# Performance work log

Measured on AMD Instinct MI355X. Metric: run time of the kernel, lower is better.

## Reference

```python
import jax, jax.numpy as jnp
import numpy as np

B, D_IN, H, C = 8192, 256, 512, 10
EXPANSION = 2
INTER = int(H * EXPANSION * 2 / 3)  # 682, matches torch int(dim*expansion*2/3)
K_OUTER, H_CYCLES, L_CYCLES = 4, 2, 3
EPS = 1e-6


def rms_norm(x):
    return x * jax.lax.rsqrt(jnp.mean(x * x, axis=-1, keepdims=True) + EPS)


def swiglu(x, Wgu, Wd):
    gate, up = jnp.split(x @ Wgu, 2, axis=-1)
    return (jax.nn.silu(gate) * up) @ Wd


def setup_inputs() -> dict:
    key = jax.random.key(0)
    ks = jax.random.split(key, 13)
    s = 0.02
    return {
        "x": jax.random.normal(ks[0], (B, D_IN), jnp.float32),
        "W_in": jax.random.normal(ks[1], (D_IN, H), jnp.float32) * s,
        "b_in": jnp.zeros((H,), jnp.float32),
        "W_fb": jax.random.normal(ks[2], (C, H), jnp.float32) * s,
        "b_fb": jnp.zeros((H,), jnp.float32),
        "Wgu1": jax.random.normal(ks[3], (H, 2 * INTER), jnp.float32) * s,
        "Wd1": jax.random.normal(ks[4], (INTER, H), jnp.float32) * s,
        "Wgu2": jax.random.normal(ks[5], (H, 2 * INTER), jnp.float32) * s,
        "Wd2": jax.random.normal(ks[6], (INTER, H), jnp.float32) * s,
        "H_init": jax.random.normal(ks[7], (H,), jnp.float32) * s,
        "L_init": jax.random.normal(ks[8], (H,), jnp.float32) * s,
        "W_out": jax.random.normal(ks[9], (H, C), jnp.float32) * s,
        "b_out": jnp.zeros((C,), jnp.float32),
    }


def reference(x, W_in, b_in, W_fb, b_fb, Wgu1, Wd1, Wgu2, Wd2,
              H_init, L_init, W_out, b_out):
    def block(h):  # TRMBlock: two post-norm SwiGLU sublayers
        h = rms_norm(h + swiglu(h, Wgu1, Wd1))
        h = rms_norm(h + swiglu(h, Wgu2, Wd2))
        return h

    def level(hidden, injection):  # TRMLevel with n_layers=1
        return block(hidden + injection)

    x_proj = x @ W_in + b_in                       # [B,H]
    z_H = jnp.broadcast_to(H_init, (x.shape[0], H))
    z_L = jnp.broadcast_to(L_init, (x.shape[0], H))
    feedback = jnp.zeros((x.shape[0], H), x.dtype)
    all_logits = []
    for k in range(K_OUTER):
        combined = x_proj + feedback
        for _h in range(H_CYCLES):
            for _l in range(L_CYCLES):
                z_L = level(z_L, z_H + combined)
            z_H = level(z_H, z_L)
        if k < K_OUTER - 1:  # grad_last_only=True: no_grad + detach
            z_H = jax.lax.stop_gradient(z_H)
            z_L = jax.lax.stop_gradient(z_L)
        logits = z_H @ W_out + b_out               # [B,C]
        all_logits.append(logits)
        probs = jax.nn.softmax(jax.lax.stop_gradient(logits), axis=-1)
        feedback = probs @ W_fb + b_fb
    return logits, jnp.stack(all_logits)
```

## Files before the change

kernel.cpp:

```cpp
#include <hip/hip_runtime.h>

#define DEVI __device__ __forceinline__

typedef __attribute__((ext_vector_type(8)))  short short8;
typedef __attribute__((ext_vector_type(4)))  short short4v;
typedef __attribute__((ext_vector_type(16))) float f32x16;

constexpr int NROW = 8192;
constexpr int HD   = 512;
constexpr int DIN  = 256;
constexpr int NC   = 10;

constexpr int NP  = 22;
constexpr int KT1 = 32;
constexpr int KT2 = 44;
constexpr int KTX = 16;
constexpr int NTH = 16;

constexpr int SZ_GU = KT1*NP*64*8;
constexpr int SZ_D  = KT2*NTH*64*8;
constexpr int SZ_IN = KTX*NTH*64*8;

DEVI short f2bf(float x){
  unsigned u = __builtin_bit_cast(unsigned, x);
  unsigned r = u + 0x7FFFu + ((u >> 16) & 1u);
  return (short)(r >> 16);
}
DEVI float bf2f(short s){
  unsigned u = ((unsigned)(unsigned short)s) << 16;
  return __builtin_bit_cast(float, u);
}
DEVI f32x16 MF(short8 a, short8 b, f32x16 c){
  return __builtin_amdgcn_mfma_f32_32x32x16_bf16(a, b, c, 0, 0, 0);
}
DEVI f32x16 fzero(){
  f32x16 v;
  #pragma unroll
  for (int i = 0; i < 16; ++i) v[i] = 0.f;
  return v;
}

struct WSet { const short *GH, *GL, *UH, *UL, *DH, *DL; };

DEVI void silu_store(int p, const f32x16& cg, const f32x16& cu,
                     short* INh_, short* INl_, int l)
{
  const int m = l & 31, g = l >> 5;
  #pragma unroll
  for (int q = 0; q < 4; ++q) {
    short4v hi, lo;
    #pragma unroll
    for (int pos = 0; pos < 4; ++pos) {
      const int r = q*4 + pos;
      float gv = cg[r], uv = cu[r];
      float sv = (gv / (1.0f + __expf(-gv))) * uv;
      short h = f2bf(sv);
      hi[pos] = h;
      lo[pos] = f2bf(sv - bf2f(h));
    }
    const int kt2  = 2*p + (q >> 1);
    const int slot = ((q & 1) << 5) + m;
    const int base = (kt2*64 + slot)*8 + (g << 2);
    *(short4v*)&INh_[base] = hi;
    *(short4v*)&INl_[base] = lo;
  }
}

template<int NPAIR>
DEVI void g1pass(int p0, const WSet& Wt,
                 const short* A1h_, const short* A1l_,
                 short* INh_, short* INl_, int l)
{
  f32x16 ag[NPAIR], au[NPAIR];
  #pragma unroll
  for (int j = 0; j < NPAIR; ++j) { ag[j] = fzero(); au[j] = fzero(); }
  const short *pGH[NPAIR], *pGL[NPAIR], *pUH[NPAIR], *pUL[NPAIR];
  #pragma unroll
  for (int j = 0; j < NPAIR; ++j) {
    const int p = p0 + 8*j;
    pGH[j] = Wt.GH + p*512 + l*8;
    pGL[j] = Wt.GL + p*512 + l*8;
    pUH[j] = Wt.UH + p*512 + l*8;
    pUL[j] = Wt.UL + p*512 + l*8;
  }
  #pragma unroll 2
  for (int kt = 0; kt < KT1; ++kt) {
    const int ab = (kt*64 + l)*8;
    short8 bh = *(const short8*)&A1h_[ab];
    short8 bl = *(const short8*)&A1l_[ab];
    const int o = kt*(NP*512);
    #pragma unroll
    for (int j = 0; j < NPAIR; ++j) {
      short8 gh = *(const short8*)(pGH[j] + o);
      short8 gl = *(const short8*)(pGL[j] + o);
      short8 uh = *(const short8*)(pUH[j] + o);
      short8 ul = *(const short8*)(pUL[j] + o);
      ag[j] = MF(gh, bh, ag[j]);
      ag[j] = MF(gl, bh, ag[j]);
      ag[j] = MF(gh, bl, ag[j]);
      au[j] = MF(uh, bh, au[j]);
      au[j] = MF(ul, bh, au[j]);
      au[j] = MF(uh, bl, au[j]);
    }
  }
  #pragma unroll
  for (int j = 0; j < NPAIR; ++j)
    silu_store(p0 + 8*j, ag[j], au[j], INh_, INl_, l);
}

DEVI void sublayer(float (&S)[32], const WSet& Wt,
                   short* A1h_, short* A1l_, short* INh_, short* INl_,
                   float* rmsS_, int w, int l)
{
  const int m = l & 31, g = l >> 5;
  #pragma unroll
  for (int t = 0; t < 2; ++t) {
    #pragma unroll
    for (int q = 0; q < 4; ++q) {
      short4v hi, lo;
      #pragma unroll
      for (int pos = 0; pos < 4; ++pos) {
        float v = S[t*16 + q*4 + pos];
        short h = f2bf(v);
        hi[pos] = h;
        lo[pos] = f2bf(v - bf2f(h));
      }
      const int kt   = 4*w + 2*t + (q >> 1);
      const int slot = ((q & 1) << 5) + m;
      const int base = (kt*64 + slot)*8 + (g << 2);
      *(short4v*)&A1h_[base] = hi;
      *(short4v*)&A1l_[base] = lo;
    }
  }
  __syncthreads();
  g1pass<2>(w, Wt, A1h_, A1l_, INh_, INl_, l);
  if (w + 16 < NP) g1pass<1>(w + 16, Wt, A1h_, A1l_, INh_, INl_, l);
  __syncthreads();
  f32x16 c0 = fzero(), c1 = fzero();
  {
    const short* d0h = Wt.DH + (2*w  )*512 + l*8;
    const short* d0l = Wt.DL + (2*w  )*512 + l*8;
    const short* d1h = Wt.DH + (2*w+1)*512 + l*8;
    const short* d1l = Wt.DL + (2*w+1)*512 + l*8;
    #pragma unroll 2
    for (int kt = 0; kt < KT2; ++kt) {
      const int ab = (kt*64 + l)*8;
      short8 bh = *(const short8*)&INh_[ab];
      short8 bl = *(const short8*)&INl_[ab];
      const int o = kt*(NTH*512);
      short8 a0h = *(const short8*)(d0h + o);
      short8 a0l = *(const short8*)(d0l + o);
      short8 a1h = *(const short8*)(d1h + o);
      short8 a1l = *(const short8*)(d1l + o);
      c0 = MF(a0h, bh, c0); c0 = MF(a0l, bh, c0); c0 = MF(a0h, bl, c0);
      c1 = MF(a1h, bh, c1); c1 = MF(a1l, bh, c1); c1 = MF(a1h, bl, c1);
    }
  }
  float ss = 0.f;
  #pragma unroll
  for (int s = 0; s < 32; ++s) {
    float y = S[s] + (s < 16 ? c0[s & 15] : c1[s & 15]);
    S[s] = y;
    ss += y*y;
  }
  ss += __shfl_xor(ss, 32);
  if (l < 32) rmsS_[w*32 + l] = ss;
  __syncthreads();
  float tot = 0.f;
  #pragma unroll
  for (int wv = 0; wv < 8; ++wv) tot += rmsS_[wv*32 + m];
  const float rinv = 1.0f / sqrtf(tot * (1.0f/512.0f) + 1e-6f);
  #pragma unroll
  for (int s = 0; s < 32; ++s) S[s] *= rinv;
}

__global__ __launch_bounds__(512, 2) void trm_main(
    const float* __restrict__ x,
    const float* __restrict__ b_in,
    const float* __restrict__ W_fb,
    const float* __restrict__ b_fb,
    const float* __restrict__ H_init,
    const float* __restrict__ L_init,
    const float* __restrict__ W_out,
    const float* __restrict__ b_out,
    float* __restrict__ xp,
    const short* __restrict__ BinH, const short* __restrict__ BinL,
    const short* __restrict__ G1H, const short* __restrict__ G1L,
    const short* __restrict__ U1H, const short* __restrict__ U1L,
    const short* __restrict__ D1H, const short* __restrict__ D1L,
    const short* __restrict__ G2H, const short* __restrict__ G2L,
    const short* __restrict__ U2H, const short* __restrict__ U2L,
    const short* __restrict__ D2H, const short* __restrict__ D2L,
    float* __restrict__ out)
{
  __shared__ alignas(16) char smem[156672];
  short* A1h  = (short*)(smem);
  short* A1l  = (short*)(smem + 32768);
  short* INh  = (short*)(smem + 65536);
  short* INl  = (short*)(smem + 110592);
  float* rmsS = (float*)(smem + 155648);
  float* lgS  = (float*)(smem);
  float* pbS  = (float*)(smem + 10240);

  const int tid = threadIdx.x;
  const int l = tid & 63;
  const int w = tid >> 6;
  const int m = l & 31;
  const int g = l >> 5;
  const int wg = blockIdx.x;
  const int row0 = wg * 32;

  float zL[32], zH[32], cb[32];

  #pragma unroll
  for (int kk = 0; kk < 2; ++kk) {
    const int kt = 2*w + kk;
    const float4* xr = (const float4*)(x + (size_t)(row0 + m)*DIN + kt*16 + g*8);
    float4 v0 = xr[0];
    float4 v1 = xr[1];
    float v[8] = {v0.x, v0.y, v0.z, v0.w, v1.x, v1.y, v1.z, v1.w};
    short8 hi, lo;
    #pragma unroll
    for (int i = 0; i < 8; ++i) {
      short h = f2bf(v[i]);
      hi[i] = h;
      lo[i] = f2bf(v[i] - bf2f(h));
    }
    const int base = (kt*64 + l)*8;
    *(short8*)&A1h[base] = hi;
    *(short8*)&A1l[base] = lo;
  }
  __syncthreads();
  {
    f32x16 c0 = fzero(), c1 = fzero();
    const short* i0h = BinH + (2*w  )*512 + l*8;
    const short* i0l = BinL + (2*w  )*512 + l*8;
    const short* i1h = BinH + (2*w+1)*512 + l*8;
    const short* i1l = BinL + (2*w+1)*512 + l*8;
    #pragma unroll 2
    for (int kt = 0; kt < KTX; ++kt) {
      const int ab = (kt*64 + l)*8;
      short8 bh = *(const short8*)&A1h[ab];
      short8 bl = *(const short8*)&A1l[ab];
      const int o = kt*(NTH*512);
      short8 a0h = *(const short8*)(i0h + o);
      short8 a0l = *(const short8*)(i0l + o);
      short8 a1h = *(const short8*)(i1h + o);
      short8 a1l = *(const short8*)(i1l + o);
      c0 = MF(a0h, bh, c0); c0 = MF(a0l, bh, c0); c0 = MF(a0h, bl, c0);
      c1 = MF(a1h, bh, c1); c1 = MF(a1l, bh, c1); c1 = MF(a1h, bl, c1);
    }
    #pragma unroll
    for (int s = 0; s < 32; ++s) {
      const int r = s & 15;
      const int cc = w*64 + (s >> 4)*32 + (r & 3) + ((r >> 2) << 3) + (g << 2);
      float v = (s < 16 ? c0[r] : c1[r]) + b_in[cc];
      cb[s] = v;
      xp[(size_t)(wg*8 + w)*2048 + s*64 + l] = v;
      zH[s] = H_init[cc];
      zL[s] = L_init[cc];
    }
  }
  __syncthreads();

  const WSet W1{G1H, G1L, U1H, U1L, D1H, D1L};
  const WSet W2{G2H, G2L, U2H, U2L, D2H, D2L};

  #pragma unroll 1
  for (int k = 0; k < 4; ++k) {
    #pragma unroll 1
    for (int hc = 0; hc < 2; ++hc) {
      #pragma unroll 1
      for (int li = 0; li < 3; ++li) {
        #pragma unroll
        for (int s = 0; s < 32; ++s) zL[s] += zH[s] + cb[s];
        #pragma unroll 1
        for (int sub = 0; sub < 2; ++sub)
          sublayer(zL, sub ? W2 : W1, A1h, A1l, INh, INl, rmsS, w, l);
      }
      #pragma unroll
      for (int s = 0; s < 32; ++s) zH[s] += zL[s];
      #pragma unroll 1
      for (int sub = 0; sub < 2; ++sub)
        sublayer(zH, sub ? W2 : W1, A1h, A1l, INh, INl, rmsS, w, l);
    }
    {
      float part[10];
      #pragma unroll
      for (int c = 0; c < NC; ++c) part[c] = 0.f;
      #pragma unroll
      for (int s = 0; s < 32; ++s) {
        const int r = s & 15;
        const int cc = w*64 + (s >> 4)*32 + (r & 3) + ((r >> 2) << 3) + (g << 2);
        const float zz = zH[s];
        #pragma unroll
        for (int c = 0; c < NC; ++c) part[c] += zz * W_out[cc*NC + c];
      }
      #pragma unroll
      for (int c = 0; c < NC; ++c) part[c] += __shfl_xor(part[c], 32);
      if (l < 32) {
        #pragma unroll
        for (int c = 0; c < NC; ++c) lgS[(w*32 + l)*NC + c] = part[c];
      }
      __syncthreads();
      if (w == 0 && l < 32) {
        float lg[10];
        #pragma unroll
        for (int c = 0; c < NC; ++c) lg[c] = b_out[c];
        #pragma unroll
        for (int wv = 0; wv < 8; ++wv) {
          #pragma unroll
          for (int c = 0; c < NC; ++c) lg[c] += lgS[(wv*32 + l)*NC + c];
        }
        const int row = row0 + l;
        #pragma unroll
        for (int c = 0; c < NC; ++c) out[(size_t)(1 + k)*81920 + row*NC + c] = lg[c];
        if (k == 3) {
          #pragma unroll
          for (int c = 0; c < NC; ++c) out[row*NC + c] = lg[c];
        }
        float mx = lg[0];
        #pragma unroll
        for (int c = 1; c < NC; ++c) mx = fmaxf(mx, lg[c]);
        float e[10], sum = 0.f;
        #pragma unroll
        for (int c = 0; c < NC; ++c) { e[c] = __expf(lg[c] - mx); sum += e[c]; }
        const float inv = 1.0f / sum;
        #pragma unroll
        for (int c = 0; c < NC; ++c) pbS[l*NC + c] = e[c] * inv;
      }
      __syncthreads();
      if (k < 3) {
        #pragma unroll
        for (int s = 0; s < 32; ++s) {
          const int r = s & 15;
          const int cc = w*64 + (s >> 4)*32 + (r & 3) + ((r >> 2) << 3) + (g << 2);
          float fb = b_fb[cc];
          #pragma unroll
          for (int c = 0; c < NC; ++c) fb += pbS[m*NC + c] * W_fb[c*HD + cc];
          cb[s] = xp[(size_t)(wg*8 + w)*2048 + s*64 + l] + fb;
        }
      }
      __syncthreads();
    }
  }
}

__global__ void prep_gu(const float* __restrict__ Wgu,
                        short* __restrict__ GH, short* __restrict__ GL,
                        short* __restrict__ UH, short* __restrict__ UL)
{
  const int t = blockIdx.x*256 + threadIdx.x;
  if (t >= 2*KT1*NP*64) return;
  const int l = t & 63;
  const int rest = t >> 6;
  const int nt = rest % NP;
  const int rest2 = rest / NP;
  const int kt = rest2 & 31;
  const int gu = rest2 >> 5;
  const int n  = nt*32 + (l & 31);
  const int kb = kt*16 + (l >> 5)*8;
  short8 hi, lo;
  #pragma unroll
  for (int i = 0; i < 8; ++i) {
    float v = 0.f;
    if (n < 682) v = Wgu[(size_t)(kb + i)*1364 + gu*682 + n];
    short h = f2bf(v);
    hi[i] = h;
    lo[i] = f2bf(v - bf2f(h));
  }
  const int base = ((kt*NP + nt)*64 + l)*8;
  short* H = gu ? UH : GH;
  short* L = gu ? UL : GL;
  *(short8*)&H[base] = hi;
  *(short8*)&L[base] = lo;
}

__global__ void prep_d(const float* __restrict__ Wd,
                       short* __restrict__ DH, short* __restrict__ DL)
{
  const int t = blockIdx.x*256 + threadIdx.x;
  if (t >= KT2*NTH*64) return;
  const int l = t & 63;
  const int rest = t >> 6;
  const int nt = rest % NTH;
  const int kt2 = rest / NTH;
  const int n  = nt*32 + (l & 31);
  const int kb = kt2*16 + (l >> 5)*8;
  short8 hi, lo;
  #pragma unroll
  for (int i = 0; i < 8; ++i) {
    const int k2 = kb + i;
    float v = (k2 < 682) ? Wd[(size_t)k2*HD + n] : 0.f;
    short h = f2bf(v);
    hi[i] = h;
    lo[i] = f2bf(v - bf2f(h));
  }
  const int base = ((kt2*NTH + nt)*64 + l)*8;
  *(short8*)&DH[base] = hi;
  *(short8*)&DL[base] = lo;
}

__global__ void prep_in(const float* __restrict__ Win,
                        short* __restrict__ IH, short* __restrict__ IL)
{
  const int t = blockIdx.x*256 + threadIdx.x;
  if (t >= KTX*NTH*64) return;
  const int l = t & 63;
  const int rest = t >> 6;
  const int nt = rest % NTH;
  const int kt = rest / NTH;
  const int n  = nt*32 + (l & 31);
  const int kb = kt*16 + (l >> 5)*8;
  short8 hi, lo;
  #pragma unroll
  for (int i = 0; i < 8; ++i) {
    float v = Win[(size_t)(kb + i)*HD + n];
    short h = f2bf(v);
    hi[i] = h;
    lo[i] = f2bf(v - bf2f(h));
  }
  const int base = ((kt*NTH + nt)*64 + l)*8;
  *(short8*)&IH[base] = hi;
  *(short8*)&IL[base] = lo;
}

extern "C" void kernel_launch(void* const* d_in, const int* in_sizes, int n_in,
                              void* d_out, int out_size, void* d_ws, size_t ws_size,
                              hipStream_t stream)
{
  const float* x     = (const float*)d_in[0];
  const float* W_in  = (const float*)d_in[1];
  const float* b_in  = (const float*)d_in[2];
  const float* W_fb  = (const float*)d_in[3];
  const float* b_fb  = (const float*)d_in[4];
  const float* Wgu1  = (const float*)d_in[5];
  const float* Wd1   = (const float*)d_in[6];
  const float* Wgu2  = (const float*)d_in[7];
  const float* Wd2   = (const float*)d_in[8];
  const float* Hini  = (const float*)d_in[9];
  const float* Lini  = (const float*)d_in[10];
  const float* W_out = (const float*)d_in[11];
  const float* b_out = (const float*)d_in[12];
  float* out = (float*)d_out;

  char* ws = (char*)d_ws;
  size_t off = 0;
  auto alloc = [&](size_t bytes) {
    char* p = ws + off;
    off = (off + bytes + 255) & ~(size_t)255;
    return p;
  };
  float* xp   = (float*)alloc((size_t)NROW*HD*4);
  short* BinH = (short*)alloc((size_t)SZ_IN*2);
  short* BinL = (short*)alloc((size_t)SZ_IN*2);
  short* G1H = (short*)alloc((size_t)SZ_GU*2); short* G1L = (short*)alloc((size_t)SZ_GU*2);
  short* U1H = (short*)alloc((size_t)SZ_GU*2); short* U1L = (short*)alloc((size_t)SZ_GU*2);
  short* D1H = (short*)alloc((size_t)SZ_D*2);  short* D1L = (short*)alloc((size_t)SZ_D*2);
  short* G2H = (short*)alloc((size_t)SZ_GU*2); short* G2L = (short*)alloc((size_t)SZ_GU*2);
  short* U2H = (short*)alloc((size_t)SZ_GU*2); short* U2L = (short*)alloc((size_t)SZ_GU*2);
  short* D2H = (short*)alloc((size_t)SZ_D*2);  short* D2L = (short*)alloc((size_t)SZ_D*2);

  const int n1 = 2*KT1*NP*64;
  prep_gu<<<(n1+255)/256, 256, 0, stream>>>(Wgu1, G1H, G1L, U1H, U1L);
  prep_gu<<<(n1+255)/256, 256, 0, stream>>>(Wgu2, G2H, G2L, U2H, U2L);
  const int n2 = KT2*NTH*64;
  prep_d<<<(n2+255)/256, 256, 0, stream>>>(Wd1, D1H, D1L);
  prep_d<<<(n2+255)/256, 256, 0, stream>>>(Wd2, D2H, D2L);
  const int n3 = KTX*NTH*64;
  prep_in<<<(n3+255)/256, 256, 0, stream>>>(W_in, BinH, BinL);

  trm_main<<<256, 512, 0, stream>>>(x, b_in, W_fb, b_fb, Hini, Lini, W_out, b_out,
      xp, BinH, BinL,
      G1H, G1L, U1H, U1L, D1H, D1L,
      G2H, G2L, U2H, U2L, D2H, D2L,
      out);
}
```

Before: 5.103 ms.

## Interleave hi/lo weight fragments and double-buffer global weight loads in MFMA loops

Weight prep now packs gate-hi, gate-lo, up-hi and up-lo fragments contiguously per lane (and hi/lo for the down and input projections), so each lane issues adjacent 16-byte loads instead of four loads from separate arrays. The K loops are rewritten with explicit register double-buffering that prefetches the next k-tile's weights while the current MFMAs run. The gate/up work split across waves changes from a 2+1 pass scheme to 3 or 2 column pairs per wave, and the two sublayers are unrolled to pass pointers directly. This targets global-load latency and address overhead in the weight-streaming GEMMs, at the cost of higher register pressure under launch_bounds(512,2).

Result: faster. 4.709 ms (-7.7%).

```diff
diff --git a/kernel.cpp b/kernel.cpp
--- a/kernel.cpp
+++ b/kernel.cpp
@@ -17,9 +17,9 @@
 constexpr int KTX = 16;
 constexpr int NTH = 16;
 
-constexpr int SZ_GU = KT1*NP*64*8;
-constexpr int SZ_D  = KT2*NTH*64*8;
-constexpr int SZ_IN = KTX*NTH*64*8;
+constexpr int SZ_P1  = KT1*NP*64*32;
+constexpr int SZ_PD  = KT2*NTH*64*16;
+constexpr int SZ_PIN = KTX*NTH*64*16;
 
 DEVI short f2bf(float x){
   unsigned u = __builtin_bit_cast(unsigned, x);
@@ -39,8 +39,6 @@
   for (int i = 0; i < 16; ++i) v[i] = 0.f;
   return v;
 }
-
-struct WSet { const short *GH, *GL, *UH, *UL, *DH, *DL; };
 
 DEVI void silu_store(int p, const f32x16& cg, const f32x16& cu,
                      short* INh_, short* INl_, int l)
@@ -67,48 +65,72 @@
 }
 
 template<int NPAIR>
-DEVI void g1pass(int p0, const WSet& Wt,
-                 const short* A1h_, const short* A1l_,
-                 short* INh_, short* INl_, int l)
-{
+DEVI void g1(const short* __restrict__ PW, int w, int l,
+             const short* __restrict__ A1h_, const short* __restrict__ A1l_,
+             short* __restrict__ INh_, short* __restrict__ INl_)
+{
+  constexpr int KSTR = NP*64*32;
   f32x16 ag[NPAIR], au[NPAIR];
   #pragma unroll
   for (int j = 0; j < NPAIR; ++j) { ag[j] = fzero(); au[j] = fzero(); }
-  const short *pGH[NPAIR], *pGL[NPAIR], *pUH[NPAIR], *pUL[NPAIR];
+  const short* base[NPAIR];
+  #pragma unroll
+  for (int j = 0; j < NPAIR; ++j)
+    base[j] = PW + ((size_t)((w + 8*j)*64 + l))*32;
+
+  short8 wa[NPAIR][4], wb[NPAIR][4];
   #pragma unroll
   for (int j = 0; j < NPAIR; ++j) {
-    const int p = p0 + 8*j;
-    pGH[j] = Wt.GH + p*512 + l*8;
-    pGL[j] = Wt.GL + p*512 + l*8;
-    pUH[j] = Wt.UH + p*512 + l*8;
-    pUL[j] = Wt.UL + p*512 + l*8;
-  }
-  #pragma unroll 2
-  for (int kt = 0; kt < KT1; ++kt) {
-    const int ab = (kt*64 + l)*8;
-    short8 bh = *(const short8*)&A1h_[ab];
-    short8 bl = *(const short8*)&A1l_[ab];
-    const int o = kt*(NP*512);
+    #pragma unroll
+    for (int i = 0; i < 4; ++i)
+      wa[j][i] = *(const short8*)(base[j] + i*8);
+  }
+
+  #pragma unroll 1
+  for (int kt = 0; kt < KT1; kt += 2) {
+    short8 bh0 = *(const short8*)&A1h_[(kt*64 + l)*8];
+    short8 bl0 = *(const short8*)&A1l_[(kt*64 + l)*8];
     #pragma unroll
     for (int j = 0; j < NPAIR; ++j) {
-      short8 gh = *(const short8*)(pGH[j] + o);
-      short8 gl = *(const short8*)(pGL[j] + o);
-      short8 uh = *(const short8*)(pUH[j] + o);
-      short8 ul = *(const short8*)(pUL[j] + o);
-      ag[j] = MF(gh, bh, ag[j]);
-      ag[j] = MF(gl, bh, ag[j]);
-      ag[j] = MF(gh, bl, ag[j]);
-      au[j] = MF(uh, bh, au[j]);
-      au[j] = MF(ul, bh, au[j]);
-      au[j] = MF(uh, bl, au[j]);
+      const short* p = base[j] + (size_t)(kt + 1)*KSTR;
+      #pragma unroll
+      for (int i = 0; i < 4; ++i) wb[j][i] = *(const short8*)(p + i*8);
+    }
+    #pragma unroll
+    for (int j = 0; j < NPAIR; ++j) {
+      ag[j] = MF(wa[j][0], bh0, ag[j]);
+      ag[j] = MF(wa[j][1], bh0, ag[j]);
+      ag[j] = MF(wa[j][0], bl0, ag[j]);
+      au[j] = MF(wa[j][2], bh0, au[j]);
+      au[j] = MF(wa[j][3], bh0, au[j]);
+      au[j] = MF(wa[j][2], bl0, au[j]);
+    }
+    short8 bh1 = *(const short8*)&A1h_[((kt+1)*64 + l)*8];
+    short8 bl1 = *(const short8*)&A1l_[((kt+1)*64 + l)*8];
+    if (kt + 2 < KT1) {
+      #pragma unroll
+      for (int j = 0; j < NPAIR; ++j) {
+        const short* p = base[j] + (size_t)(kt + 2)*KSTR;
+        #pragma unroll
+        for (int i = 0; i < 4; ++i) wa[j][i] = *(const short8*)(p + i*8);
+      }
+    }
+    #pragma unroll
+    for (int j = 0; j < NPAIR; ++j) {
+      ag[j] = MF(wb[j][0], bh1, ag[j]);
+      ag[j] = MF(wb[j][1], bh1, ag[j]);
+      ag[j] = MF(wb[j][0], bl1, ag[j]);
+      au[j] = MF(wb[j][2], bh1, au[j]);
+      au[j] = MF(wb[j][3], bh1, au[j]);
+      au[j] = MF(wb[j][2], bl1, au[j]);
     }
   }
   #pragma unroll
   for (int j = 0; j < NPAIR; ++j)
-    silu_store(p0 + 8*j, ag[j], au[j], INh_, INl_, l);
-}
-
-DEVI void sublayer(float (&S)[32], const WSet& Wt,
+    silu_store(w + 8*j, ag[j], au[j], INh_, INl_, l);
+}
+
+DEVI void sublayer(float (&S)[32], const short* __restrict__ PW, const short* __restrict__ PD,
                    short* A1h_, short* A1l_, short* INh_, short* INl_,
                    float* rmsS_, int w, int l)
 {
@@ -133,27 +155,42 @@
     }
   }
   __syncthreads();
-  g1pass<2>(w, Wt, A1h_, A1l_, INh_, INl_, l);
-  if (w + 16 < NP) g1pass<1>(w + 16, Wt, A1h_, A1l_, INh_, INl_, l);
+  if (w < 6) g1<3>(PW, w, l, A1h_, A1l_, INh_, INl_);
+  else       g1<2>(PW, w, l, A1h_, A1l_, INh_, INl_);
   __syncthreads();
   f32x16 c0 = fzero(), c1 = fzero();
   {
-    const short* d0h = Wt.DH + (2*w  )*512 + l*8;
-    const short* d0l = Wt.DL + (2*w  )*512 + l*8;
-    const short* d1h = Wt.DH + (2*w+1)*512 + l*8;
-    const short* d1l = Wt.DL + (2*w+1)*512 + l*8;
-    #pragma unroll 2
-    for (int kt = 0; kt < KT2; ++kt) {
-      const int ab = (kt*64 + l)*8;
-      short8 bh = *(const short8*)&INh_[ab];
-      short8 bl = *(const short8*)&INl_[ab];
-      const int o = kt*(NTH*512);
-      short8 a0h = *(const short8*)(d0h + o);
-      short8 a0l = *(const short8*)(d0l + o);
-      short8 a1h = *(const short8*)(d1h + o);
-      short8 a1l = *(const short8*)(d1l + o);
-      c0 = MF(a0h, bh, c0); c0 = MF(a0l, bh, c0); c0 = MF(a0h, bl, c0);
-      c1 = MF(a1h, bh, c1); c1 = MF(a1l, bh, c1); c1 = MF(a1h, bl, c1);
+    constexpr int DSTR = NTH*64*16;
+    const short* bD = PD + ((size_t)(2*w*64 + l))*16;
+    short8 da0 = *(const short8*)(bD);
+    short8 da1 = *(const short8*)(bD + 8);
+    short8 da2 = *(const short8*)(bD + 1024);
+    short8 da3 = *(const short8*)(bD + 1032);
+    short8 db0, db1, db2, db3;
+    #pragma unroll 1
+    for (int kt = 0; kt < KT2; kt += 2) {
+      short8 bh0 = *(const short8*)&INh_[(kt*64 + l)*8];
+      short8 bl0 = *(const short8*)&INl_[(kt*64 + l)*8];
+      {
+        const short* p = bD + (size_t)(kt + 1)*DSTR;
+        db0 = *(const short8*)(p);
+        db1 = *(const short8*)(p + 8);
+        db2 = *(const short8*)(p + 1024);
+        db3 = *(const short8*)(p + 1032);
+      }
+      c0 = MF(da0, bh0, c0); c0 = MF(da1, bh0, c0); c0 = MF(da0, bl0, c0);
+      c1 = MF(da2, bh0, c1); c1 = MF(da3, bh0, c1); c1 = MF(da2, bl0, c1);
+      short8 bh1 = *(const short8*)&INh_[((kt+1)*64 + l)*8];
+      short8 bl1 = *(const short8*)&INl_[((kt+1)*64 + l)*8];
+      if (kt + 2 < KT2) {
+        const short* p = bD + (size_t)(kt + 2)*DSTR;
+        da0 = *(const short8*)(p);
+        da1 = *(const short8*)(p + 8);
+        da2 = *(const short8*)(p + 1024);
+        da3 = *(const short8*)(p + 1032);
+      }
+      c0 = MF(db0, bh1, c0); c0 = MF(db1, bh1, c0); c0 = MF(db0, bl1, c0);
+      c1 = MF(db2, bh1, c1); c1 = MF(db3, bh1, c1); c1 = MF(db2, bl1, c1);
     }
   }
   float ss = 0.f;
@@ -184,13 +221,9 @@
     const float* __restrict__ W_out,
     const float* __restrict__ b_out,
     float* __restrict__ xp,
-    const short* __restrict__ BinH, const short* __restrict__ BinL,
-    const short* __restrict__ G1H, const short* __restrict__ G1L,
-    const short* __restrict__ U1H, const short* __restrict__ U1L,
-    const short* __restrict__ D1H, const short* __restrict__ D1L,
-    const short* __restrict__ G2H, const short* __restrict__ G2L,
-    const short* __restrict__ U2H, const short* __restrict__ U2L,
-    const short* __restrict__ D2H, const short* __restrict__ D2L,
+    const short* __restrict__ PIN,
+    const short* __restrict__ P1, const short* __restrict__ PD1,
+    const short* __restrict__ P2, const short* __restrict__ PD2,
     float* __restrict__ out)
 {
   __shared__ alignas(16) char smem[156672];
@@ -233,22 +266,37 @@
   __syncthreads();
   {
     f32x16 c0 = fzero(), c1 = fzero();
-    const short* i0h = BinH + (2*w  )*512 + l*8;
-    const short* i0l = BinL + (2*w  )*512 + l*8;
-    const short* i1h = BinH + (2*w+1)*512 + l*8;
-    const short* i1l = BinL + (2*w+1)*512 + l*8;
-    #pragma unroll 2
-    for (int kt = 0; kt < KTX; ++kt) {
-      const int ab = (kt*64 + l)*8;
-      short8 bh = *(const short8*)&A1h[ab];
-      short8 bl = *(const short8*)&A1l[ab];
-      const int o = kt*(NTH*512);
-      short8 a0h = *(const short8*)(i0h + o);
-      short8 a0l = *(const short8*)(i0l + o);
-      short8 a1h = *(const short8*)(i1h + o);
-      short8 a1l = *(const short8*)(i1l + o);
-      c0 = MF(a0h, bh, c0); c0 = MF(a0l, bh, c0); c0 = MF(a0h, bl, c0);
-      c1 = MF(a1h, bh, c1); c1 = MF(a1l, bh, c1); c1 = MF(a1h, bl, c1);
+    constexpr int ISTR = NTH*64*16;
+    const short* bI = PIN + ((size_t)(2*w*64 + l))*16;
+    short8 da0 = *(const short8*)(bI);
+    short8 da1 = *(const short8*)(bI + 8);
+    short8 da2 = *(const short8*)(bI + 1024);
+    short8 da3 = *(const short8*)(bI + 1032);
+    short8 db0, db1, db2, db3;
+    #pragma unroll 1
+    for (int kt = 0; kt < KTX; kt += 2) {
+      short8 bh0 = *(const short8*)&A1h[(kt*64 + l)*8];
+      short8 bl0 = *(const short8*)&A1l[(kt*64 + l)*8];
+      {
+        const short* p = bI + (size_t)(kt + 1)*ISTR;
+        db0 = *(const short8*)(p);
+        db1 = *(const short8*)(p + 8);
+        db2 = *(const short8*)(p + 1024);
+        db3 = *(const short8*)(p + 1032);
+      }
+      c0 = MF(da0, bh0, c0); c0 = MF(da1, bh0, c0); c0 = MF(da0, bl0, c0);
+      c1 = MF(da2, bh0, c1); c1 = MF(da3, bh0, c1); c1 = MF(da2, bl0, c1);
+      short8 bh1 = *(const short8*)&A1h[((kt+1)*64 + l)*8];
+      short8 bl1 = *(const short8*)&A1l[((kt+1)*64 + l)*8];
+      if (kt + 2 < KTX) {
+        const short* p = bI + (size_t)(kt + 2)*ISTR;
+        da0 = *(const short8*)(p);
+        da1 = *(const short8*)(p + 8);
+        da2 = *(const short8*)(p + 1024);
+        da3 = *(const short8*)(p + 1032);
+      }
+      c0 = MF(db0, bh1, c0); c0 = MF(db1, bh1, c0); c0 = MF(db0, bl1, c0);
+      c1 = MF(db2, bh1, c1); c1 = MF(db3, bh1, c1); c1 = MF(db2, bl1, c1);
     }
     #pragma unroll
     for (int s = 0; s < 32; ++s) {
@@ -263,9 +311,6 @@
   }
   __syncthreads();
 
-  const WSet W1{G1H, G1L, U1H, U1L, D1H, D1L};
-  const WSet W2{G2H, G2L, U2H, U2L, D2H, D2L};
-
   #pragma unroll 1
   for (int k = 0; k < 4; ++k) {
     #pragma unroll 1
@@ -274,15 +319,13 @@
       for (int li = 0; li < 3; ++li) {
         #pragma unroll
         for (int s = 0; s < 32; ++s) zL[s] += zH[s] + cb[s];
-        #pragma unroll 1
-        for (int sub = 0; sub < 2; ++sub)
-          sublayer(zL, sub ? W2 : W1, A1h, A1l, INh, INl, rmsS, w, l);
+        sublayer(zL, P1, PD1, A1h, A1l, INh, INl, rmsS, w, l);
+        sublayer(zL, P2, PD2, A1h, A1l, INh, INl, rmsS, w, l);
       }
       #pragma unroll
       for (int s = 0; s < 32; ++s) zH[s] += zL[s];
-      #pragma unroll 1
-      for (int sub = 0; sub < 2; ++sub)
-        sublayer(zH, sub ? W2 : W1, A1h, A1l, INh, INl, rmsS, w, l);
+      sublayer(zH, P1, PD1, A1h, A1l, INh, INl, rmsS, w, l);
+      sublayer(zH, P2, PD2, A1h, A1l, INh, INl, rmsS, w, l);
     }
     {
       float part[10];
@@ -346,38 +389,35 @@
   }
 }
 
-__global__ void prep_gu(const float* __restrict__ Wgu,
-                        short* __restrict__ GH, short* __restrict__ GL,
-                        short* __restrict__ UH, short* __restrict__ UL)
+__global__ void prep_gu(const float* __restrict__ Wgu, short* __restrict__ P)
 {
   const int t = blockIdx.x*256 + threadIdx.x;
-  if (t >= 2*KT1*NP*64) return;
+  if (t >= KT1*NP*64) return;
   const int l = t & 63;
   const int rest = t >> 6;
   const int nt = rest % NP;
-  const int rest2 = rest / NP;
-  const int kt = rest2 & 31;
-  const int gu = rest2 >> 5;
+  const int kt = rest / NP;
   const int n  = nt*32 + (l & 31);
   const int kb = kt*16 + (l >> 5)*8;
-  short8 hi, lo;
+  short8 gh8, gl8, uh8, ul8;
   #pragma unroll
   for (int i = 0; i < 8; ++i) {
-    float v = 0.f;
-    if (n < 682) v = Wgu[(size_t)(kb + i)*1364 + gu*682 + n];
-    short h = f2bf(v);
-    hi[i] = h;
-    lo[i] = f2bf(v - bf2f(h));
-  }
-  const int base = ((kt*NP + nt)*64 + l)*8;
-  short* H = gu ? UH : GH;
-  short* L = gu ? UL : GL;
-  *(short8*)&H[base] = hi;
-  *(short8*)&L[base] = lo;
-}
-
-__global__ void prep_d(const float* __restrict__ Wd,
-                       short* __restrict__ DH, short* __restrict__ DL)
+    float gv = 0.f, uv = 0.f;
+    if (n < 682) {
+      gv = Wgu[(size_t)(kb + i)*1364 + n];
+      uv = Wgu[(size_t)(kb + i)*1364 + 682 + n];
+    }
+    short gh = f2bf(gv); gh8[i] = gh; gl8[i] = f2bf(gv - bf2f(gh));
+    short uh = f2bf(uv); uh8[i] = uh; ul8[i] = f2bf(uv - bf2f(uh));
+  }
+  short* dst = P + ((size_t)(kt*NP + nt)*64 + l)*32;
+  *(short8*)(dst)      = gh8;
+  *(short8*)(dst + 8)  = gl8;
+  *(short8*)(dst + 16) = uh8;
+  *(short8*)(dst + 24) = ul8;
+}
+
+__global__ void prep_d(const float* __restrict__ Wd, short* __restrict__ P)
 {
   const int t = blockIdx.x*256 + threadIdx.x;
   if (t >= KT2*NTH*64) return;
@@ -387,22 +427,19 @@
   const int kt2 = rest / NTH;
   const int n  = nt*32 + (l & 31);
   const int kb = kt2*16 + (l >> 5)*8;
-  short8 hi, lo;
+  short8 h8, l8;
   #pragma unroll
   for (int i = 0; i < 8; ++i) {
     const int k2 = kb + i;
     float v = (k2 < 682) ? Wd[(size_t)k2*HD + n] : 0.f;
-    short h = f2bf(v);
-    hi[i] = h;
-    lo[i] = f2bf(v - bf2f(h));
-  }
-  const int base = ((kt2*NTH + nt)*64 + l)*8;
-  *(short8*)&DH[base] = hi;
-  *(short8*)&DL[base] = lo;
-}
-
-__global__ void prep_in(const float* __restrict__ Win,
-                        short* __restrict__ IH, short* __restrict__ IL)
+    short h = f2bf(v); h8[i] = h; l8[i] = f2bf(v - bf2f(h));
+  }
+  short* dst = P + ((size_t)(kt2*NTH + nt)*64 + l)*16;
+  *(short8*)(dst)     = h8;
+  *(short8*)(dst + 8) = l8;
+}
+
+__global__ void prep_in(const float* __restrict__ Win, short* __restrict__ P)
 {
   const int t = blockIdx.x*256 + threadIdx.x;
   if (t >= KTX*NTH*64) return;
@@ -412,17 +449,15 @@
   const int kt = rest / NTH;
   const int n  = nt*32 + (l & 31);
   const int kb = kt*16 + (l >> 5)*8;
-  short8 hi, lo;
+  short8 h8, l8;
   #pragma unroll
   for (int i = 0; i < 8; ++i) {
     float v = Win[(size_t)(kb + i)*HD + n];
-    short h = f2bf(v);
-    hi[i] = h;
-    lo[i] = f2bf(v - bf2f(h));
-  }
-  const int base = ((kt*NTH + nt)*64 + l)*8;
-  *(short8*)&IH[base] = hi;
-  *(short8*)&IL[base] = lo;
+    short h = f2bf(v); h8[i] = h; l8[i] = f2bf(v - bf2f(h));
+  }
+  short* dst = P + ((size_t)(kt*NTH + nt)*64 + l)*16;
+  *(short8*)(dst)     = h8;
+  *(short8*)(dst + 8) = l8;
 }
 
 extern "C" void kernel_launch(void* const* d_in, const int* in_sizes, int n_in,
@@ -451,28 +486,22 @@
     off = (off + bytes + 255) & ~(size_t)255;
     return p;
   };
-  float* xp   = (float*)alloc((size_t)NROW*HD*4);
-  short* BinH = (short*)alloc((size_t)SZ_IN*2);
-  short* BinL = (short*)alloc((size_t)SZ_IN*2);
-  short* G1H = (short*)alloc((size_t)SZ_GU*2); short* G1L = (short*)alloc((size_t)SZ_GU*2);
-  short* U1H = (short*)alloc((size_t)SZ_GU*2); short* U1L = (short*)alloc((size_t)SZ_GU*2);
-  short* D1H = (short*)alloc((size_t)SZ_D*2);  short* D1L = (short*)alloc((size_t)SZ_D*2);
-  short* G2H = (short*)alloc((size_t)SZ_GU*2); short* G2L = (short*)alloc((size_t)SZ_GU*2);
-  short* U2H = (short*)alloc((size_t)SZ_GU*2); short* U2L = (short*)alloc((size_t)SZ_GU*2);
-  short* D2H = (short*)alloc((size_t)SZ_D*2);  short* D2L = (short*)alloc((size_t)SZ_D*2);
-
-  const int n1 = 2*KT1*NP*64;
-  prep_gu<<<(n1+255)/256, 256, 0, stream>>>(Wgu1, G1H, G1L, U1H, U1L);
-  prep_gu<<<(n1+255)/256, 256, 0, stream>>>(Wgu2, G2H, G2L, U2H, U2L);
+  float* xp  = (float*)alloc((size_t)NROW*HD*4);
+  short* PIN = (short*)alloc((size_t)SZ_PIN*2);
+  short* P1  = (short*)alloc((size_t)SZ_P1*2);
+  short* PD1 = (short*)alloc((size_t)SZ_PD*2);
+  short* P2  = (short*)alloc((size_t)SZ_P1*2);
+  short* PD2 = (short*)alloc((size_t)SZ_PD*2);
+
+  const int n1 = KT1*NP*64;
+  prep_gu<<<(n1+255)/256, 256, 0, stream>>>(Wgu1, P1);
+  prep_gu<<<(n1+255)/256, 256, 0, stream>>>(Wgu2, P2);
   const int n2 = KT2*NTH*64;
-  prep_d<<<(n2+255)/256, 256, 0, stream>>>(Wd1, D1H, D1L);
-  prep_d<<<(n2+255)/256, 256, 0, stream>>>(Wd2, D2H, D2L);
+  prep_d<<<(n2+255)/256, 256, 0, stream>>>(Wd1, PD1);
+  prep_d<<<(n2+255)/256, 256, 0, stream>>>(Wd2, PD2);
   const int n3 = KTX*NTH*64;
-  prep_in<<<(n3+255)/256, 256, 0, stream>>>(W_in, BinH, BinL);
+  prep_in<<<(n3+255)/256, 256, 0, stream>>>(W_in, PIN);
 
   trm_main<<<256, 512, 0, stream>>>(x, b_in, W_fb, b_fb, Hini, Lini, W_out, b_out,
-      xp, BinH, BinL,
-      G1H, G1L, U1H, U1L, D1H, D1L,
-      G2H, G2L, U2H, U2L, D2H, D2L,
-      out);
-}
+      xp, PIN, P1, PD1, P2, PD2, out);
+}
```
